# Optimization experiments

Hardware: AMD Instinct MI355X
Metric: run time of the kernel (lower is better)

## Reference

```python
import jax, jax.numpy as jnp
import numpy as np

B, S, H = 4, 8192, 576
I = 512   # moe_intermediate_size
E = 8     # num routed experts
TOP_K = 2

def setup_inputs() -> dict:
    key = jax.random.key(0)
    ks = jax.random.split(key, 8)
    sc = lambda fan_in: 1.0 / np.sqrt(fan_in)
    return {
        'x': jax.random.normal(ks[0], (B, S, H), dtype=jnp.float32),
        'shared_gate_w': jax.random.normal(ks[1], (H, I), dtype=jnp.float32) * sc(H),
        'shared_up_w':   jax.random.normal(ks[2], (H, I), dtype=jnp.float32) * sc(H),
        'shared_down_w': jax.random.normal(ks[3], (I, H), dtype=jnp.float32) * sc(I),
        'routed_gate_w': jax.random.normal(ks[4], (E, H, I), dtype=jnp.float32) * sc(H),
        'routed_up_w':   jax.random.normal(ks[5], (E, H, I), dtype=jnp.float32) * sc(H),
        'routed_down_w': jax.random.normal(ks[6], (E, I, H), dtype=jnp.float32) * sc(I),
        'router_w':      jax.random.normal(ks[7], (H, E), dtype=jnp.float32) * sc(H),
        'router_bias':   jnp.zeros((E,), dtype=jnp.float32),
    }

def reference(x, shared_gate_w, shared_up_w, shared_down_w,
              routed_gate_w, routed_up_w, routed_down_w,
              router_w, router_bias):
    b, s, h = x.shape
    flat = x.reshape(-1, h)                               # [T, H]
    T = flat.shape[0]

    # shared expert (SwiGLU)
    shared = (jax.nn.silu(flat @ shared_gate_w) * (flat @ shared_up_w)) @ shared_down_w

    # router: softmax over experts, top-k, renormalize, scatter back to dense weights
    router_logits = flat @ router_w + router_bias          # [T, E]
    routing_weights = jax.nn.softmax(router_logits, axis=1)
    topk_w, topk_i = jax.lax.top_k(routing_weights, TOP_K)  # [T, k]
    topk_w = topk_w / jnp.sum(topk_w, axis=-1, keepdims=True)
    expert_weights = jnp.zeros((T, routing_weights.shape[1]), dtype=routing_weights.dtype)
    expert_weights = expert_weights.at[jnp.arange(T)[:, None], topk_i].set(topk_w)

    # dense all-expert SwiGLU (faithful to reference: every token through every expert)
    gate = jnp.einsum('th,ehi->tei', flat, routed_gate_w)   # [T, E, I]
    up   = jnp.einsum('th,ehi->tei', flat, routed_up_w)
    expert_out = jnp.einsum('tei,eih->teh', jax.nn.silu(gate) * up, routed_down_w)  # [T, E, H]

    weighted = jnp.einsum('teh,te->th', expert_out, expert_weights)
    return (shared + weighted).reshape(b, s, h)
```

## Files before the change

kernel.cpp:

```cpp
#include <hip/hip_runtime.h>
#include <stdint.h>

#define T_TOK 32768
#define H_DIM 576
#define I_DIM 512
#define NEXP 8
#define WELEM 294912

typedef __attribute__((ext_vector_type(8))) short short8;
typedef __attribute__((ext_vector_type(4))) float f32x4;
typedef __attribute__((ext_vector_type(4))) float f4;
typedef __attribute__((ext_vector_type(4))) unsigned short u16x4;

__device__ __forceinline__ unsigned short f2bf(float f) {
  union { float f; unsigned u; } v; v.f = f;
  unsigned r = (v.u + 0x7fffu + ((v.u >> 16) & 1u)) >> 16;
  return (unsigned short)r;
}

__device__ __forceinline__ void gl16(const void* g, void* l) {
  __builtin_amdgcn_global_load_lds(
      (const __attribute__((address_space(1))) unsigned*)g,
      (__attribute__((address_space(3))) unsigned*)l, 16, 0, 0);
}

__global__ __launch_bounds__(256) void routercvt_k(
    const float* __restrict__ x, unsigned short* __restrict__ xb,
    const float* __restrict__ rw, const float* __restrict__ rb,
    int* __restrict__ tki, float* __restrict__ tkw, int* __restrict__ counts) {
  __shared__ float lrw[H_DIM * NEXP];
  __shared__ float tile[32][132];
  __shared__ float red[128][8];
  __shared__ int hist[16];
  int tid = threadIdx.x;
  for (int i = tid; i < 1152; i += 256)
    *(f4*)&lrw[i * 4] = *(const f4*)&rw[i * 4];
  if (tid < 16) hist[tid] = 0;
  int t0 = blockIdx.x * 128;
  int half = tid >> 7, tl = tid & 127;
  float acc[NEXP] = {};
  for (int c = 0; c < 18; c++) {
    __syncthreads();
#pragma unroll
    for (int k = 0; k < 4; k++) {
      int f = tid + k * 256;
      int rgrp = f >> 9, fl = f & 511;
      int tl2 = fl >> 2, seg = fl & 3;
      int h = (rgrp ? 288 : 0) + c * 16 + seg * 4;
      size_t gi = (size_t)(t0 + tl2) * H_DIM + h;
      f4 v = *(const f4*)(x + gi);
      u16x4 o;
      o.x = f2bf(v.x); o.y = f2bf(v.y); o.z = f2bf(v.z); o.w = f2bf(v.w);
      *(u16x4*)(xb + gi) = o;
      int row = rgrp * 16 + seg * 4;
      tile[row + 0][tl2] = v.x; tile[row + 1][tl2] = v.y;
      tile[row + 2][tl2] = v.z; tile[row + 3][tl2] = v.w;
    }
    __syncthreads();
    int hbase = half * 288 + c * 16;
    int rbase = half * 16;
#pragma unroll
    for (int hh = 0; hh < 16; hh++) {
      float xv = tile[rbase + hh][tl];
      f4 w0 = *(const f4*)&lrw[(hbase + hh) * 8];
      f4 w1 = *(const f4*)&lrw[(hbase + hh) * 8 + 4];
      acc[0] += xv * w0.x; acc[1] += xv * w0.y;
      acc[2] += xv * w0.z; acc[3] += xv * w0.w;
      acc[4] += xv * w1.x; acc[5] += xv * w1.y;
      acc[6] += xv * w1.z; acc[7] += xv * w1.w;
    }
  }
  if (half) {
#pragma unroll
    for (int e = 0; e < NEXP; e++) red[tl][e] = acc[e];
  }
  __syncthreads();
  if (!half) {
    int t = t0 + tl;
    float l[NEXP];
#pragma unroll
    for (int e = 0; e < NEXP; e++) l[e] = acc[e] + red[tl][e] + rb[e];
    int e0 = 0;
#pragma unroll
    for (int e = 1; e < NEXP; e++) if (l[e] > l[e0]) e0 = e;
    int e1 = -1;
#pragma unroll
    for (int e = 0; e < NEXP; e++) {
      if (e == e0) continue;
      if (e1 < 0 || l[e] > l[e1]) e1 = e;
    }
    float w0 = 1.f / (1.f + __expf(l[e1] - l[e0]));
    tki[t * 2] = e0; tki[t * 2 + 1] = e1;
    tkw[t * 2] = w0; tkw[t * 2 + 1] = 1.f - w0;
    atomicAdd(&hist[e0], 1);
    atomicAdd(&hist[8 + e1], 1);
  }
  __syncthreads();
  if (tid < 16) atomicAdd(&counts[tid * 32], hist[tid]);
}

__global__ void cvt_w_k(const float* __restrict__ sgw, const float* __restrict__ suw,
                        const float* __restrict__ rgw, const float* __restrict__ ruw,
                        const float* __restrict__ sdw, const float* __restrict__ rdw,
                        unsigned short* __restrict__ wsg, unsigned short* __restrict__ wsu,
                        unsigned short* __restrict__ wrg, unsigned short* __restrict__ wru,
                        unsigned short* __restrict__ wsd, unsigned short* __restrict__ wrd) {
  __shared__ float tile[32][33];
  int b = blockIdx.x;
  const float* src; unsigned short* dst;
  int C, bx, by;
  if (b < 5184) {
    int z = b / 288, r = b % 288;
    bx = r & 15; by = r >> 4; C = 512;
    if (z == 0)      { src = sgw;                            dst = wsg; }
    else if (z == 1) { src = suw;                            dst = wsu; }
    else if (z < 10) { src = rgw + (size_t)(z - 2) * WELEM;  dst = wrg + (size_t)(z - 2) * WELEM; }
    else             { src = ruw + (size_t)(z - 10) * WELEM; dst = wru + (size_t)(z - 10) * WELEM; }
  } else {
    int b2 = b - 5184;
    int z = b2 / 288, r = b2 % 288;
    bx = r % 18; by = r / 18; C = 576;
    src = (z == 0) ? sdw : rdw + (size_t)(z - 1) * WELEM;
    dst = (z == 0) ? wsd : wrd + (size_t)(z - 1) * WELEM;
  }
  int R = 1088 - C;
  int r0 = by * 32, c0 = bx * 32;
  for (int i = threadIdx.y; i < 32; i += 8)
    tile[i][threadIdx.x] = src[(size_t)(r0 + i) * C + c0 + threadIdx.x];
  __syncthreads();
  for (int i = threadIdx.y; i < 32; i += 8)
    dst[(size_t)(c0 + i) * R + r0 + threadIdx.x] = f2bf(tile[threadIdx.x][i]);
}

__global__ void offsets_k(const int* __restrict__ counts, int* __restrict__ offs16,
                          int* __restrict__ pcnt16, int* __restrict__ pinfo) {
  if (threadIdx.x == 0) {
    int o = 0;
    for (int s = 0; s < 16; s++) {
      int c = counts[s * 32];
      int pc = (c + 127) & ~127;
      offs16[s] = o; pcnt16[s] = pc;
      o += pc;
    }
    pinfo[0] = offs16[8];
    pinfo[1] = o - offs16[8];
  }
}

__global__ __launch_bounds__(256) void scatter_k(
    const int* __restrict__ tki, const float* __restrict__ tkw,
    const int* __restrict__ offs16, int* __restrict__ cursor ,
    int* __restrict__ etok, float* __restrict__ ew) {
  __shared__ int hist[16], base[16], lcur[16];
  int tid = threadIdx.x;
  if (tid < 16) { hist[tid] = 0; lcur[tid] = 0; }
  __syncthreads();
  int t = blockIdx.x * 256 + tid;
  int s0 = tki[t * 2], s1 = 8 + tki[t * 2 + 1];
  atomicAdd(&hist[s0], 1);
  atomicAdd(&hist[s1], 1);
  __syncthreads();
  if (tid < 16) base[tid] = atomicAdd(&cursor[tid * 32], hist[tid]);
  __syncthreads();
#pragma unroll
  for (int k = 0; k < 2; k++) {
    int s = (k == 0) ? s0 : s1;
    int r = atomicAdd(&lcur[s], 1);
    int slot = offs16[s] + base[s] + r;
    etok[slot] = t;
    ew[slot] = tkw[t * 2 + k];
  }
}

template <int SHARED>
__global__ __launch_bounds__(512, 2) void gateup_k(
    const unsigned short* __restrict__ xb, const unsigned short* __restrict__ wg,
    const unsigned short* __restrict__ wu, unsigned short* __restrict__ h,
    const int* __restrict__ etok, const int* __restrict__ offs16,
    const int* __restrict__ pcnt16, const int* __restrict__ pinfo,
    int p, int merged, int mchunk) {
  int bid = blockIdx.x;
  int xcd = bid & 7, l = bid >> 3;
  int mb = xcd * mchunk + (l >> 2);
  int nb = l & 3;
  int nrows = SHARED ? T_TOK : (merged ? pinfo[0] + pinfo[1] : pinfo[p]);
  if (mb * 128 >= nrows) return;
  __shared__ unsigned short As[128 * 32];
  __shared__ unsigned short Bg[128 * 32];
  __shared__ unsigned short Bu[128 * 32];
  int t = threadIdx.x;
  int wv = t >> 6, lane = t & 63;
  int ar = t >> 2, seg = t & 3;
  int sg = seg ^ ((ar >> 1) & 3);
  int m0 = mb * 128 + ar;
  int tok0, e = 0;
  if (SHARED) {
    tok0 = m0;
  } else {
    int rl = (!merged && p) ? pinfo[0] : 0;
    int g = rl + m0;
    int s = 0;
#pragma unroll
    for (int i = 0; i < 15; i++) s += (g >= offs16[i] + pcnt16[i]) ? 1 : 0;
    e = s & 7;
    tok0 = etok[g];
    if (tok0 < 0) tok0 = 0;
  }
  const unsigned short* ga = xb + (size_t)tok0 * H_DIM + sg * 8;
  int n0 = nb * 128 + ar;
  const unsigned short* gg = wg + (size_t)e * WELEM + (size_t)n0 * H_DIM + sg * 8;
  const unsigned short* gu = wu + (size_t)e * WELEM + (size_t)n0 * H_DIM + sg * 8;
  char* lA = (char*)As + wv * 1024;
  char* lG = (char*)Bg + wv * 1024;
  char* lU = (char*)Bu + wv * 1024;
  int fr = lane & 15, fq = lane >> 4;
  int wm = (wv >> 2) * 64, wn = (wv & 3) * 32;
  f32x4 accg[4][2] = {};
  f32x4 accu[4][2] = {};
  for (int k0 = 0; k0 < H_DIM; k0 += 32) {
    gl16(ga + k0, lA);
    gl16(gg + k0, lG);
    gl16(gu + k0, lU);
    __syncthreads();
    short8 a[4], g[2], u[2];
#pragma unroll
    for (int i = 0; i < 4; i++) {
      int r = wm + i * 16 + fr;
      a[i] = *(const short8*)&As[r * 32 + (fq ^ ((r >> 1) & 3)) * 8];
    }
#pragma unroll
    for (int j = 0; j < 2; j++) {
      int r = wn + j * 16 + fr;
      int sw = (fq ^ ((r >> 1) & 3)) * 8;
      g[j] = *(const short8*)&Bg[r * 32 + sw];
      u[j] = *(const short8*)&Bu[r * 32 + sw];
    }
#pragma unroll
    for (int i = 0; i < 4; i++)
#pragma unroll
      for (int j = 0; j < 2; j++) {
        accg[i][j] = __builtin_amdgcn_mfma_f32_16x16x32_bf16(a[i], g[j], accg[i][j], 0, 0, 0);
        accu[i][j] = __builtin_amdgcn_mfma_f32_16x16x32_bf16(a[i], u[j], accu[i][j], 0, 0, 0);
      }
    __syncthreads();
  }
#pragma unroll
  for (int i = 0; i < 4; i++)
#pragma unroll
    for (int j = 0; j < 2; j++)
#pragma unroll
      for (int r = 0; r < 4; r++) {
        int row = mb * 128 + wm + i * 16 + fq * 4 + r;
        int col = nb * 128 + wn + j * 16 + fr;
        float gv = accg[i][j][r], uv = accu[i][j][r];
        float hv = (gv / (1.f + __expf(-gv))) * uv;
        h[(size_t)row * I_DIM + col] = f2bf(hv);
      }
}

template <int MODE>
__global__ __launch_bounds__(512, 2) void down_k(
    const unsigned short* __restrict__ hbuf, const unsigned short* __restrict__ wd,
    float* __restrict__ out, const int* __restrict__ etok, const float* __restrict__ ew,
    const int* __restrict__ offs16, const int* __restrict__ pcnt16,
    const int* __restrict__ pinfo, int p, int merged, int mchunk) {
  int bid = blockIdx.x;
  int xcd = bid & 7, l = bid >> 3;
  int mb = xcd * mchunk + l / 5;
  int nb = l % 5;
  int nrows = (MODE == 0) ? T_TOK : pinfo[p];
  if (mb * 128 >= nrows) return;
  int row_lo = (MODE == 1 && p == 1) ? pinfo[0] : 0;
  int hrow_lo = (MODE == 1 && merged) ? row_lo : 0;
  __shared__ unsigned short AB[2][128 * 32];
  int t = threadIdx.x;
  int wv = t >> 6, lane = t & 63;
  int ar = t >> 2, seg = t & 3;
  int sg = seg ^ ((ar >> 1) & 3);
  int e = 0;
  if (MODE == 1) {
    int g = row_lo + mb * 128 + ar;
    int s = 0;
#pragma unroll
    for (int i = 0; i < 15; i++) s += (g >= offs16[i] + pcnt16[i]) ? 1 : 0;
    e = s & 7;
  }
  const unsigned short* ga = hbuf + (size_t)(hrow_lo + mb * 128 + ar) * I_DIM + sg * 8;
  int n0 = nb * 128 + ar;
  if (n0 > H_DIM - 1) n0 = H_DIM - 1;
  const unsigned short* gb = wd + (size_t)e * WELEM + (size_t)n0 * I_DIM + sg * 8;
  char* lA = (char*)AB[0] + wv * 1024;
  char* lB = (char*)AB[1] + wv * 1024;
  int fr = lane & 15, fq = lane >> 4;
  int wm = (wv >> 2) * 64, wn = (wv & 3) * 32;
  f32x4 acc[4][2] = {};
  for (int k0 = 0; k0 < I_DIM; k0 += 32) {
    gl16(ga + k0, lA);
    gl16(gb + k0, lB);
    __syncthreads();
    short8 a[4], b2[2];
#pragma unroll
    for (int i = 0; i < 4; i++) {
      int r = wm + i * 16 + fr;
      a[i] = *(const short8*)&AB[0][r * 32 + (fq ^ ((r >> 1) & 3)) * 8];
    }
#pragma unroll
    for (int j = 0; j < 2; j++) {
      int r = wn + j * 16 + fr;
      b2[j] = *(const short8*)&AB[1][r * 32 + (fq ^ ((r >> 1) & 3)) * 8];
    }
#pragma unroll
    for (int i = 0; i < 4; i++)
#pragma unroll
      for (int j = 0; j < 2; j++)
        acc[i][j] = __builtin_amdgcn_mfma_f32_16x16x32_bf16(a[i], b2[j], acc[i][j], 0, 0, 0);
    __syncthreads();
  }
  float* st = (float*)AB;
  int q = t & 31;
  int colv = nb * 128 + q * 4;
  bool colok = colv < H_DIM;
#pragma unroll
  for (int c = 0; c < 4; c++) {
    __syncthreads();
    if ((wm == 64) == (c >= 2)) {
#pragma unroll
      for (int ii = 0; ii < 2; ii++) {
        int i = (c & 1) * 2 + ii;
#pragma unroll
        for (int j = 0; j < 2; j++)
#pragma unroll
          for (int r = 0; r < 4; r++)
            st[(ii * 16 + fq * 4 + r) * 128 + wn + j * 16 + fr] = acc[i][j][r];
      }
    }
    __syncthreads();
#pragma unroll
    for (int ps = 0; ps < 2; ps++) {
      int lr = (t >> 5) + ps * 16;
      int mloc = mb * 128 + c * 32 + lr;
      if (colok) {
        f4 v = *(f4*)&st[lr * 128 + q * 4];
        if (MODE == 0) {
          *(f4*)&out[(size_t)mloc * H_DIM + colv] = v;
        } else {
          int g = row_lo + mloc;
          int tok = etok[g];
          if (tok >= 0) {
            float w = ew[g];
            float* op = &out[(size_t)tok * H_DIM + colv];
            f4 o = *(f4*)op;
            o.x += w * v.x; o.y += w * v.y; o.z += w * v.z; o.w += w * v.w;
            *(f4*)op = o;
          }
        }
      }
    }
  }
}


extern "C" void kernel_launch(void* const* d_in, const int* in_sizes, int n_in,
                              void* d_out, int out_size, void* d_ws, size_t ws_size,
                              hipStream_t stream) {
  const float* x = (const float*)d_in[0];
  const float* sgw = (const float*)d_in[1];
  const float* suw = (const float*)d_in[2];
  const float* sdw = (const float*)d_in[3];
  const float* rgw = (const float*)d_in[4];
  const float* ruw = (const float*)d_in[5];
  const float* rdw = (const float*)d_in[6];
  const float* rw = (const float*)d_in[7];
  const float* rb = (const float*)d_in[8];
  float* out = (float*)d_out;
  char* ws = (char*)d_ws;

  const size_t o_xb = 0;
  const size_t o_w = 37748736;
  const size_t w_sg = o_w;
  const size_t w_su = o_w + 589824;
  const size_t w_sd = o_w + 1179648;
  const size_t w_rg = o_w + 1769472;
  const size_t w_ru = o_w + 6488064;
  const size_t w_rd = o_w + 11206656;
  const size_t o_tki = o_w + 15925248;
  const size_t o_tkw = o_tki + 262144;
  const size_t o_meta = o_tkw + 262144;
  const size_t o_etok = o_meta + 8192;
  const size_t o_ew = o_etok + 270336;
  const size_t o_h = o_ew + 270336;
  const size_t need_merged = o_h + (size_t)67584 * 1024;

  unsigned short* xb = (unsigned short*)(ws + o_xb);
  int* tki = (int*)(ws + o_tki);
  float* tkw = (float*)(ws + o_tkw);
  int* counts = (int*)(ws + o_meta);
  int* cursor = counts + 512;
  int* offs16 = counts + 1024;
  int* pcnt16 = counts + 1040;
  int* pinfo = counts + 1056;
  int* etok = (int*)(ws + o_etok);
  float* ew = (float*)(ws + o_ew);
  unsigned short* h = (unsigned short*)(ws + o_h);
  int merged = (ws_size >= need_merged) ? 1 : 0;

  unsigned short* wsg = (unsigned short*)(ws + w_sg);
  unsigned short* wsu = (unsigned short*)(ws + w_su);
  unsigned short* wsd = (unsigned short*)(ws + w_sd);
  unsigned short* wrg = (unsigned short*)(ws + w_rg);
  unsigned short* wru = (unsigned short*)(ws + w_ru);
  unsigned short* wrd = (unsigned short*)(ws + w_rd);

  hipMemsetAsync(ws + o_meta, 0, 8192, stream);
  hipMemsetAsync(etok, 0xFF, 270336, stream);

  routercvt_k<<<256, 256, 0, stream>>>(x, xb, rw, rb, tki, tkw, counts);
  cvt_w_k<<<7776, dim3(32, 8), 0, stream>>>(sgw, suw, rgw, ruw, sdw, rdw,
                                            wsg, wsu, wrg, wru, wsd, wrd);
  offsets_k<<<1, 64, 0, stream>>>(counts, offs16, pcnt16, pinfo);
  scatter_k<<<128, 256, 0, stream>>>(tki, tkw, offs16, cursor, etok, ew);

  gateup_k<1><<<1024, 512, 0, stream>>>(xb, wsg, wsu, h, nullptr, nullptr,
                                        nullptr, nullptr, 0, 0, 32);
  down_k<0><<<1280, 512, 0, stream>>>(h, wsd, out, nullptr, nullptr, nullptr,
                                      nullptr, nullptr, 0, 0, 32);

  if (merged) {
    gateup_k<0><<<2112, 512, 0, stream>>>(xb, wrg, wru, h, etok, offs16,
                                          pcnt16, pinfo, 0, 1, 66);
    down_k<1><<<1320, 512, 0, stream>>>(h, wrd, out, etok, ew, offs16,
                                        pcnt16, pinfo, 0, 1, 33);
    down_k<1><<<1320, 512, 0, stream>>>(h, wrd, out, etok, ew, offs16,
                                        pcnt16, pinfo, 1, 1, 33);
  } else {
    for (int p = 0; p < 2; p++) {
      gateup_k<0><<<1056, 512, 0, stream>>>(xb, wrg, wru, h, etok, offs16,
                                            pcnt16, pinfo, p, 0, 33);
      down_k<1><<<1320, 512, 0, stream>>>(h, wrd, out, etok, ew, offs16,
                                          pcnt16, pinfo, p, 0, 33);
    }
  }
}
```

Before: 344.7 us.

## Double-buffer gate/up LDS loads and widen down-proj N tile to 192

The gate/up kernel now double-buffers its LDS tiles, issuing the next K-slice's global-to-LDS loads before computing on the current slice and dropping one barrier per iteration. The down-projection kernel switches from 5 padded 128-column tiles to 3 exact 192-column tiles covering H=576, with each wave computing 3 MFMA column blocks. This removes the wasted padded columns and reduces how often the A operand is re-read, at the cost of more LDS and accumulator registers per block and fewer blocks. The gate/up loop still ends each iteration with a barrier but has none between issuing a prefetch and reading it in the next iteration, so correctness depends on the load completing by then.

Result: slower. 365.5 us (+6.0%).

```diff
diff --git a/kernel.cpp b/kernel.cpp
--- a/kernel.cpp
+++ b/kernel.cpp
@@ -185,9 +185,9 @@
   int nb = l & 3;
   int nrows = SHARED ? T_TOK : (merged ? pinfo[0] + pinfo[1] : pinfo[p]);
   if (mb * 128 >= nrows) return;
-  __shared__ unsigned short As[128 * 32];
-  __shared__ unsigned short Bg[128 * 32];
-  __shared__ unsigned short Bu[128 * 32];
+  __shared__ unsigned short As[2][4096];
+  __shared__ unsigned short Bg[2][4096];
+  __shared__ unsigned short Bu[2][4096];
   int t = threadIdx.x;
   int wv = t >> 6, lane = t & 63;
   int ar = t >> 2, seg = t & 3;
@@ -210,30 +210,36 @@
   int n0 = nb * 128 + ar;
   const unsigned short* gg = wg + (size_t)e * WELEM + (size_t)n0 * H_DIM + sg * 8;
   const unsigned short* gu = wu + (size_t)e * WELEM + (size_t)n0 * H_DIM + sg * 8;
-  char* lA = (char*)As + wv * 1024;
-  char* lG = (char*)Bg + wv * 1024;
-  char* lU = (char*)Bu + wv * 1024;
+  int wb = wv * 1024;
   int fr = lane & 15, fq = lane >> 4;
   int wm = (wv >> 2) * 64, wn = (wv & 3) * 32;
   f32x4 accg[4][2] = {};
   f32x4 accu[4][2] = {};
-  for (int k0 = 0; k0 < H_DIM; k0 += 32) {
-    gl16(ga + k0, lA);
-    gl16(gg + k0, lG);
-    gl16(gu + k0, lU);
-    __syncthreads();
+  gl16(ga, (char*)As[0] + wb);
+  gl16(gg, (char*)Bg[0] + wb);
+  gl16(gu, (char*)Bu[0] + wb);
+  __syncthreads();
+  const int NS = H_DIM / 32;
+  for (int s = 0; s < NS; s++) {
+    int cur = s & 1;
+    if (s + 1 < NS) {
+      int k1 = (s + 1) * 32;
+      gl16(ga + k1, (char*)As[cur ^ 1] + wb);
+      gl16(gg + k1, (char*)Bg[cur ^ 1] + wb);
+      gl16(gu + k1, (char*)Bu[cur ^ 1] + wb);
+    }
     short8 a[4], g[2], u[2];
 #pragma unroll
     for (int i = 0; i < 4; i++) {
       int r = wm + i * 16 + fr;
-      a[i] = *(const short8*)&As[r * 32 + (fq ^ ((r >> 1) & 3)) * 8];
+      a[i] = *(const short8*)&As[cur][r * 32 + (fq ^ ((r >> 1) & 3)) * 8];
     }
 #pragma unroll
     for (int j = 0; j < 2; j++) {
       int r = wn + j * 16 + fr;
       int sw = (fq ^ ((r >> 1) & 3)) * 8;
-      g[j] = *(const short8*)&Bg[r * 32 + sw];
-      u[j] = *(const short8*)&Bu[r * 32 + sw];
+      g[j] = *(const short8*)&Bg[cur][r * 32 + sw];
+      u[j] = *(const short8*)&Bu[cur][r * 32 + sw];
     }
 #pragma unroll
     for (int i = 0; i < 4; i++)
@@ -266,13 +272,15 @@
     const int* __restrict__ pinfo, int p, int merged, int mchunk) {
   int bid = blockIdx.x;
   int xcd = bid & 7, l = bid >> 3;
-  int mb = xcd * mchunk + l / 5;
-  int nb = l % 5;
+  int mb = xcd * mchunk + l / 3;
+  int nb = l % 3;
   int nrows = (MODE == 0) ? T_TOK : pinfo[p];
   if (mb * 128 >= nrows) return;
   int row_lo = (MODE == 1 && p == 1) ? pinfo[0] : 0;
   int hrow_lo = (MODE == 1 && merged) ? row_lo : 0;
-  __shared__ unsigned short AB[2][128 * 32];
+  __shared__ char lds[24576];
+  unsigned short* Ab = (unsigned short*)lds;
+  unsigned short* Bb = (unsigned short*)(lds + 8192);
   int t = threadIdx.x;
   int wv = t >> 6, lane = t & 63;
   int ar = t >> 2, seg = t & 3;
@@ -286,40 +294,37 @@
     e = s & 7;
   }
   const unsigned short* ga = hbuf + (size_t)(hrow_lo + mb * 128 + ar) * I_DIM + sg * 8;
-  int n0 = nb * 128 + ar;
-  if (n0 > H_DIM - 1) n0 = H_DIM - 1;
-  const unsigned short* gb = wd + (size_t)e * WELEM + (size_t)n0 * I_DIM + sg * 8;
-  char* lA = (char*)AB[0] + wv * 1024;
-  char* lB = (char*)AB[1] + wv * 1024;
+  int n00 = nb * 192 + ar;
+  const unsigned short* gb0 = wd + (size_t)e * WELEM + (size_t)n00 * I_DIM + sg * 8;
+  const unsigned short* gb1 = gb0 + (size_t)128 * I_DIM;
+  int wb = wv * 1024;
   int fr = lane & 15, fq = lane >> 4;
-  int wm = (wv >> 2) * 64, wn = (wv & 3) * 32;
-  f32x4 acc[4][2] = {};
+  int wm = (wv >> 2) * 64, wn = (wv & 3) * 48;
+  f32x4 acc[4][3] = {};
   for (int k0 = 0; k0 < I_DIM; k0 += 32) {
-    gl16(ga + k0, lA);
-    gl16(gb + k0, lB);
-    __syncthreads();
-    short8 a[4], b2[2];
+    gl16(ga + k0, (char*)Ab + wb);
+    gl16(gb0 + k0, (char*)Bb + wb);
+    if (t < 256) gl16(gb1 + k0, (char*)Bb + 8192 + wb);
+    __syncthreads();
+    short8 a[4], b2[3];
 #pragma unroll
     for (int i = 0; i < 4; i++) {
       int r = wm + i * 16 + fr;
-      a[i] = *(const short8*)&AB[0][r * 32 + (fq ^ ((r >> 1) & 3)) * 8];
-    }
-#pragma unroll
-    for (int j = 0; j < 2; j++) {
+      a[i] = *(const short8*)&Ab[r * 32 + (fq ^ ((r >> 1) & 3)) * 8];
+    }
+#pragma unroll
+    for (int j = 0; j < 3; j++) {
       int r = wn + j * 16 + fr;
-      b2[j] = *(const short8*)&AB[1][r * 32 + (fq ^ ((r >> 1) & 3)) * 8];
+      b2[j] = *(const short8*)&Bb[r * 32 + (fq ^ ((r >> 1) & 3)) * 8];
     }
 #pragma unroll
     for (int i = 0; i < 4; i++)
 #pragma unroll
-      for (int j = 0; j < 2; j++)
+      for (int j = 0; j < 3; j++)
         acc[i][j] = __builtin_amdgcn_mfma_f32_16x16x32_bf16(a[i], b2[j], acc[i][j], 0, 0, 0);
     __syncthreads();
   }
-  float* st = (float*)AB;
-  int q = t & 31;
-  int colv = nb * 128 + q * 4;
-  bool colok = colv < H_DIM;
+  float* st = (float*)lds;
 #pragma unroll
   for (int c = 0; c < 4; c++) {
     __syncthreads();
@@ -328,31 +333,31 @@
       for (int ii = 0; ii < 2; ii++) {
         int i = (c & 1) * 2 + ii;
 #pragma unroll
-        for (int j = 0; j < 2; j++)
+        for (int j = 0; j < 3; j++)
 #pragma unroll
           for (int r = 0; r < 4; r++)
-            st[(ii * 16 + fq * 4 + r) * 128 + wn + j * 16 + fr] = acc[i][j][r];
+            st[(ii * 16 + fq * 4 + r) * 192 + wn + j * 16 + fr] = acc[i][j][r];
       }
     }
     __syncthreads();
 #pragma unroll
-    for (int ps = 0; ps < 2; ps++) {
-      int lr = (t >> 5) + ps * 16;
+    for (int i2 = 0; i2 < 3; i2++) {
+      int s = t + i2 * 512;
+      int lr = s / 48, qq = s % 48;
       int mloc = mb * 128 + c * 32 + lr;
-      if (colok) {
-        f4 v = *(f4*)&st[lr * 128 + q * 4];
-        if (MODE == 0) {
-          *(f4*)&out[(size_t)mloc * H_DIM + colv] = v;
-        } else {
-          int g = row_lo + mloc;
-          int tok = etok[g];
-          if (tok >= 0) {
-            float w = ew[g];
-            float* op = &out[(size_t)tok * H_DIM + colv];
-            f4 o = *(f4*)op;
-            o.x += w * v.x; o.y += w * v.y; o.z += w * v.z; o.w += w * v.w;
-            *(f4*)op = o;
-          }
+      int colv = nb * 192 + qq * 4;
+      f4 v = *(f4*)&st[lr * 192 + qq * 4];
+      if (MODE == 0) {
+        *(f4*)&out[(size_t)mloc * H_DIM + colv] = v;
+      } else {
+        int g = row_lo + mloc;
+        int tok = etok[g];
+        if (tok >= 0) {
+          float w = ew[g];
+          float* op = &out[(size_t)tok * H_DIM + colv];
+          f4 o = *(f4*)op;
+          o.x += w * v.x; o.y += w * v.y; o.z += w * v.z; o.w += w * v.w;
+          *(f4*)op = o;
         }
       }
     }
@@ -422,22 +427,22 @@
 
   gateup_k<1><<<1024, 512, 0, stream>>>(xb, wsg, wsu, h, nullptr, nullptr,
                                         nullptr, nullptr, 0, 0, 32);
-  down_k<0><<<1280, 512, 0, stream>>>(h, wsd, out, nullptr, nullptr, nullptr,
-                                      nullptr, nullptr, 0, 0, 32);
+  down_k<0><<<768, 512, 0, stream>>>(h, wsd, out, nullptr, nullptr, nullptr,
+                                     nullptr, nullptr, 0, 0, 32);
 
   if (merged) {
     gateup_k<0><<<2112, 512, 0, stream>>>(xb, wrg, wru, h, etok, offs16,
                                           pcnt16, pinfo, 0, 1, 66);
-    down_k<1><<<1320, 512, 0, stream>>>(h, wrd, out, etok, ew, offs16,
-                                        pcnt16, pinfo, 0, 1, 33);
-    down_k<1><<<1320, 512, 0, stream>>>(h, wrd, out, etok, ew, offs16,
-                                        pcnt16, pinfo, 1, 1, 33);
+    down_k<1><<<792, 512, 0, stream>>>(h, wrd, out, etok, ew, offs16,
+                                       pcnt16, pinfo, 0, 1, 33);
+    down_k<1><<<792, 512, 0, stream>>>(h, wrd, out, etok, ew, offs16,
+                                       pcnt16, pinfo, 1, 1, 33);
   } else {
     for (int p = 0; p < 2; p++) {
       gateup_k<0><<<1056, 512, 0, stream>>>(xb, wrg, wru, h, etok, offs16,
                                             pcnt16, pinfo, p, 0, 33);
-      down_k<1><<<1320, 512, 0, stream>>>(h, wrd, out, etok, ew, offs16,
-                                          pcnt16, pinfo, p, 0, 33);
-    }
-  }
-}
+      down_k<1><<<792, 512, 0, stream>>>(h, wrd, out, etok, ew, offs16,
+                                         pcnt16, pinfo, p, 0, 33);
+    }
+  }
+}
```
